# Performance work log

Measured on AMD Instinct MI355X. Metric: run time of the kernel, lower is better.

The kernel has to match this reference:

```python
import jax, jax.numpy as jnp
import numpy as np

DIM = 1028


def setup_inputs() -> dict:
    key = jax.random.key(0)
    ks = jax.random.split(key, 11)
    B, N = 8, 2048
    s = 0.02
    x = jax.random.normal(ks[0], (B, N, DIM), dtype=jnp.float32)
    Wq = jax.random.normal(ks[1], (DIM, DIM), dtype=jnp.float32) * s
    bq = jax.random.normal(ks[2], (DIM,), dtype=jnp.float32) * s
    Wk = jax.random.normal(ks[3], (DIM, DIM), dtype=jnp.float32) * s
    bk = jax.random.normal(ks[4], (DIM,), dtype=jnp.float32) * s
    Wv = jax.random.normal(ks[5], (DIM, DIM), dtype=jnp.float32) * s
    bv = jax.random.normal(ks[6], (DIM,), dtype=jnp.float32) * s
    We = jax.random.normal(ks[7], (4 * DIM, DIM), dtype=jnp.float32) * s
    be = jax.random.normal(ks[8], (4 * DIM,), dtype=jnp.float32) * s
    Wo = jax.random.normal(ks[9], (DIM, 4 * DIM), dtype=jnp.float32) * s
    bo = jax.random.normal(ks[10], (DIM,), dtype=jnp.float32) * s
    return {"x": x, "Wq": Wq, "bq": bq, "Wk": Wk, "bk": bk, "Wv": Wv,
            "bv": bv, "We": We, "be": be, "Wo": Wo, "bo": bo}


def reference(x, Wq, bq, Wk, bk, Wv, bv, We, be, Wo, bo):
    # x: [B, N, D]. torch Linear weight is [out, in] -> x @ W.T + b
    q = jnp.einsum('bnd,ed->bne', x, Wq) + bq
    k = jnp.einsum('bnd,ed->bne', x, Wk) + bk
    v = jnp.einsum('bnd,ed->bne', x, Wv) + bv
    scores = jnp.einsum('bqd,bkd->bqk', q, k) / jnp.sqrt(jnp.float32(DIM))
    w = jax.nn.softmax(scores, axis=-1)          # [B, N, N]
    attn = jnp.einsum('bqk,bkd->bqd', w, v)      # [B, N, D]
    h = jax.nn.gelu(jnp.einsum('bnd,hd->bnh', attn, We) + be, approximate=False)
    out = jnp.einsum('bnh,dh->bnd', h, Wo) + bo
    return out + x
```

## Files before the change

### kernel.cpp

```cpp
#include <hip/hip_runtime.h>
#include <hip/hip_bf16.h>
#include <cstdint>
#include <cmath>


typedef __bf16 bf16;
typedef __bf16 bf16x8 __attribute__((ext_vector_type(8)));
typedef float  f32x4  __attribute__((ext_vector_type(4)));

#define D_REAL   1028
#define D_PADK   1088
#define D_PADN   1152
#define H_REAL   4112
#define H_PAD    4224
#define NTOK     2048
#define NB       8
#define MTOT     (NB*NTOK)
#define SLAB_X   ((size_t)NTOK*D_PADK)
#define SLAB_S   ((size_t)NTOK*NTOK)
#define WSLAB    ((size_t)D_PADN*D_PADK)
#define VSLAB    ((size_t)D_PADN*NTOK)

__device__ __forceinline__ void async16(const void* g, void* l) {
    __builtin_amdgcn_global_load_lds(
        (__attribute__((address_space(1))) void*)(uintptr_t)g,
        (__attribute__((address_space(3))) void*)(uint32_t)(uintptr_t)l,
        16, 0, 0);
}

template <int EPI, bool XPIN>
__global__ __launch_bounds__(256)
void gemm_bt(const bf16* __restrict__ A, size_t strideA,
             const bf16* __restrict__ B, size_t strideB,
             const float* __restrict__ bias, size_t strideBias,
             void* __restrict__ Out, size_t strideOut,
             bf16* __restrict__ OutV,
             int K, int outPitch, int colBound, float scale,
             const float* __restrict__ resid)
{
    __shared__ __attribute__((aligned(16))) bf16 tA[128 * 64];
    __shared__ __attribute__((aligned(16))) bf16 tB[128 * 64];

    int bx, by, bz;
    if (XPIN) { bz = blockIdx.x; by = blockIdx.y; bx = blockIdx.z; }
    else      { bx = blockIdx.x; by = blockIdx.y; bz = blockIdx.z; }

    A += (size_t)bz * strideA;
    B += (size_t)bz * strideB;
    if (bias) bias += (size_t)bz * strideBias;

    const int tid  = threadIdx.x;
    const int lane = tid & 63;
    const int wv   = tid >> 6;
    const int wm   = wv >> 1;
    const int wn   = wv & 1;

    f32x4 acc[4][4] = {};

    const int sRow = lane >> 3;
    const int sCh  = (lane & 7) ^ sRow;
    const bf16* gA = A + (size_t)(by * 128 + wv * 32 + sRow) * K + sCh * 8;
    const bf16* gB = B + (size_t)(bx * 128 + wv * 32 + sRow) * K + sCh * 8;
    bf16* lA = &tA[(wv * 32) * 64];
    bf16* lB = &tB[(wv * 32) * 64];

    const int lr  = lane & 15;
    const int lq  = lane >> 4;
    const int rsw = lr & 7;

    for (int k0 = 0; k0 < K; k0 += 64) {
        async16(gA,                  lA);
        async16(gA + (size_t) 8 * K, lA +  8 * 64);
        async16(gA + (size_t)16 * K, lA + 16 * 64);
        async16(gA + (size_t)24 * K, lA + 24 * 64);
        async16(gB,                  lB);
        async16(gB + (size_t) 8 * K, lB +  8 * 64);
        async16(gB + (size_t)16 * K, lB + 16 * 64);
        async16(gB + (size_t)24 * K, lB + 24 * 64);
        gA += 64; gB += 64;
        __syncthreads();

        #pragma unroll
        for (int kk = 0; kk < 2; ++kk) {
            const int sl = ((kk * 4 + lq) ^ rsw) << 3;
            bf16x8 af[4], bfr[4];
            #pragma unroll
            for (int i = 0; i < 4; ++i) {
                af[i]  = *(const bf16x8*)&tA[(wm * 64 + i * 16 + lr) * 64 + sl];
                bfr[i] = *(const bf16x8*)&tB[(wn * 64 + i * 16 + lr) * 64 + sl];
            }
            #pragma unroll
            for (int i = 0; i < 4; ++i)
                #pragma unroll
                for (int j = 0; j < 4; ++j)
                    acc[i][j] = __builtin_amdgcn_mfma_f32_16x16x32_bf16(
                        af[i], bfr[j], acc[i][j], 0, 0, 0);
        }
        __syncthreads();
    }

    #pragma unroll
    for (int i = 0; i < 4; ++i) {
        #pragma unroll
        for (int j = 0; j < 4; ++j) {
            f32x4 v = acc[i][j];
            const int cg = bx * 128 + wn * 64 + j * 16 + lr;
            if (cg >= colBound) continue;
            const int rowBase = by * 128 + wm * 64 + i * 16 + lq * 4;
            const float bs = bias ? bias[cg] : 0.0f;
            #pragma unroll
            for (int r = 0; r < 4; ++r) {
                const int mg = rowBase + r;
                const float val = v[r];
                if (EPI == 0) {
                    ((bf16*)Out + (size_t)bz * strideOut)[(size_t)mg * outPitch + cg] =
                        (bf16)(val + bs);
                } else if (EPI == 3) {
                    const float u = val + bs;
                    const float g = 0.5f * u * (1.0f + erff(u * 0.70710678118654752f));
                    ((bf16*)Out)[(size_t)mg * outPitch + cg] = (bf16)g;
                } else if (EPI == 4) {
                    ((float*)Out)[(size_t)mg * outPitch + cg] =
                        val + bs + resid[(size_t)mg * outPitch + cg];
                } else if (EPI == 5) {
                    const int grp = cg / D_PADN;
                    const int c   = cg - grp * D_PADN;
                    const float u = val + bs;
                    if (grp < 2) {
                        if (c < D_PADK)
                            ((bf16*)Out)[(size_t)bz * 2 * SLAB_X + (size_t)grp * SLAB_X +
                                         (size_t)mg * D_PADK + c] = (bf16)u;
                    } else {
                        OutV[(size_t)bz * VSLAB + (size_t)c * NTOK + mg] = (bf16)u;
                    }
                } else {
                    ((bf16*)Out + (size_t)bz * strideOut)[(size_t)mg * outPitch + cg] =
                        (bf16)(val * scale);
                }
            }
        }
    }
}

__global__ __launch_bounds__(256)
void cvt_pad(const float* __restrict__ src, int R, int C,
             bf16* __restrict__ dst, int CP)
{
    const int c = blockIdx.x * 256 + threadIdx.x;
    const int r = blockIdx.y;
    if (c >= CP) return;
    const float v = (r < R && c < C) ? src[(size_t)r * C + c] : 0.0f;
    dst[(size_t)r * CP + c] = (bf16)v;
}

__global__ __launch_bounds__(256)
void pad_bias(const float* __restrict__ src, int n, float* __restrict__ dst, int np)
{
    const int i = blockIdx.x * 256 + threadIdx.x;
    if (i < np) dst[i] = (i < n) ? src[i] : 0.0f;
}

__global__ __launch_bounds__(256)
void softmax_ip(bf16* __restrict__ S)
{
    const int row  = blockIdx.x * 4 + (threadIdx.x >> 6);
    const int lane = threadIdx.x & 63;
    bf16* s = S + (size_t)row * NTOK + lane * 8;

    float v[32];
    #pragma unroll
    for (int j = 0; j < 4; ++j) {
        bf16x8 t = *(const bf16x8*)(s + j * 512);
        #pragma unroll
        for (int e = 0; e < 8; ++e) v[j * 8 + e] = (float)t[e];
    }
    float m = -1e30f;
    #pragma unroll
    for (int i = 0; i < 32; ++i) m = fmaxf(m, v[i]);
    #pragma unroll
    for (int off = 32; off > 0; off >>= 1) m = fmaxf(m, __shfl_xor(m, off, 64));

    float sum = 0.0f;
    #pragma unroll
    for (int i = 0; i < 32; ++i) { v[i] = __expf(v[i] - m); sum += v[i]; }
    #pragma unroll
    for (int off = 32; off > 0; off >>= 1) sum += __shfl_xor(sum, off, 64);
    const float inv = 1.0f / sum;

    #pragma unroll
    for (int j = 0; j < 4; ++j) {
        bf16x8 t;
        #pragma unroll
        for (int e = 0; e < 8; ++e) t[e] = (bf16)(v[j * 8 + e] * inv);
        *(bf16x8*)(s + j * 512) = t;
    }
}

#define OFF_WQKV   0u
#define OFF_WE     7520256u
#define OFF_WO     16711680u
#define OFF_BQKV   26443776u
#define OFF_BE     26457600u
#define OFF_XBF    26474496u
#define OFF_VT     62126080u
#define OFF_SCR    99874816u
#define QS_BYTES   8912896u
#define SS_BYTES   8388608u

extern "C" void kernel_launch(void* const* d_in, const int* in_sizes, int n_in,
                              void* d_out, int out_size, void* d_ws, size_t ws_size,
                              hipStream_t stream)
{
    const float* x  = (const float*)d_in[0];
    const float* Wq = (const float*)d_in[1];
    const float* bq = (const float*)d_in[2];
    const float* Wk = (const float*)d_in[3];
    const float* bk = (const float*)d_in[4];
    const float* Wv = (const float*)d_in[5];
    const float* bv = (const float*)d_in[6];
    const float* We = (const float*)d_in[7];
    const float* be = (const float*)d_in[8];
    const float* Wo = (const float*)d_in[9];
    const float* bo = (const float*)d_in[10];

    char* ws = (char*)d_ws;
    bf16*  Wqkv = (bf16*)(ws + OFF_WQKV);
    bf16*  WeP  = (bf16*)(ws + OFF_WE);
    bf16*  WoP  = (bf16*)(ws + OFF_WO);
    float* Bqkv = (float*)(ws + OFF_BQKV);
    float* BeP  = (float*)(ws + OFF_BE);
    bf16*  Xbf  = (bf16*)(ws + OFF_XBF);
    bf16*  Vt   = (bf16*)(ws + OFF_VT);
    char*  scr  = ws + OFF_SCR;

    const size_t avail = ws_size > OFF_SCR ? ws_size - OFF_SCR : 0;
    const size_t perG  = (size_t)QS_BYTES + SS_BYTES;
    int G = (avail >= 8 * perG) ? 8 : (avail >= 4 * perG) ? 4
          : (avail >= 2 * perG) ? 2 : 1;
    int R = (avail >= 69206016u) ? 8192 : (avail >= 34603008u) ? 4096 : 2048;

    bf16* Qs = (bf16*)scr;
    bf16* Ss = (bf16*)(scr + (size_t)G * QS_BYTES);
    bf16* Hb = (bf16*)scr;

    const dim3 blk(256);
    const float inv_sqrt_d = (float)(1.0 / sqrt((double)D_REAL));

    cvt_pad<<<dim3(5, MTOT), blk, 0, stream>>>(x, MTOT, D_REAL, Xbf, D_PADK);
    cvt_pad<<<dim3(5, D_PADN), blk, 0, stream>>>(Wq, D_REAL, D_REAL, Wqkv, D_PADK);
    cvt_pad<<<dim3(5, D_PADN), blk, 0, stream>>>(Wk, D_REAL, D_REAL, Wqkv + WSLAB, D_PADK);
    cvt_pad<<<dim3(5, D_PADN), blk, 0, stream>>>(Wv, D_REAL, D_REAL, Wqkv + 2 * WSLAB, D_PADK);
    cvt_pad<<<dim3(5, H_PAD), blk, 0, stream>>>(We, H_REAL, D_REAL, WeP, D_PADK);
    cvt_pad<<<dim3(17, D_PADN), blk, 0, stream>>>(Wo, D_REAL, H_REAL, WoP, H_PAD);
    pad_bias<<<dim3(5), blk, 0, stream>>>(bq, D_REAL, Bqkv, D_PADN);
    pad_bias<<<dim3(5), blk, 0, stream>>>(bk, D_REAL, Bqkv + D_PADN, D_PADN);
    pad_bias<<<dim3(5), blk, 0, stream>>>(bv, D_REAL, Bqkv + 2 * D_PADN, D_PADN);
    pad_bias<<<dim3(17), blk, 0, stream>>>(be, H_REAL, BeP, H_PAD);

    for (int g0 = 0; g0 < NB; g0 += G) {
        gemm_bt<5, false><<<dim3(27, 16, G), blk, 0, stream>>>(
            Xbf + (size_t)g0 * SLAB_X, SLAB_X, Wqkv, 0, Bqkv, 0,
            Qs, 0, Vt + (size_t)g0 * VSLAB,
            D_PADK, 0, 3456, 1.0f, nullptr);
        gemm_bt<6, true><<<dim3(G, 16, 16), blk, 0, stream>>>(
            Qs, 2 * SLAB_X, Qs + SLAB_X, 2 * SLAB_X, nullptr, 0,
            Ss, SLAB_S, nullptr, D_PADK, NTOK, NTOK, inv_sqrt_d, nullptr);
        softmax_ip<<<dim3(G * 512), blk, 0, stream>>>(Ss);
        gemm_bt<0, true><<<dim3(G, 16, 9), blk, 0, stream>>>(
            Ss, SLAB_S, Vt + (size_t)g0 * VSLAB, VSLAB, nullptr, 0,
            Xbf + (size_t)g0 * SLAB_X, SLAB_X, nullptr,
            NTOK, D_PADK, D_PADK, 1.0f, nullptr);
    }

    for (int r0 = 0; r0 < MTOT; r0 += R) {
        gemm_bt<3, false><<<dim3(33, R / 128, 1), blk, 0, stream>>>(
            Xbf + (size_t)r0 * D_PADK, 0, WeP, 0, BeP, 0,
            Hb, 0, nullptr, D_PADK, H_PAD, H_PAD, 1.0f, nullptr);
        gemm_bt<4, false><<<dim3(9, R / 128, 1), blk, 0, stream>>>(
            Hb, 0, WoP, 0, bo, 0,
            (float*)d_out + (size_t)r0 * D_REAL, 0, nullptr,
            H_PAD, D_REAL, D_REAL, 1.0f, x + (size_t)r0 * D_REAL);
    }
}
```

Baseline: 1.071 ms.

## Fuse softmax into score and PV GEMMs and remap blocks across XCDs

Removes the separate softmax pass. The QK^T GEMM now writes exp(scaled score) directly and atomically accumulates per-row sums, and the PV GEMM divides by the row sum in its epilogue. This avoids reading and writing the full score matrix once more. It also flattens all grids to 1D with a remap that groups contiguous logical tiles onto the same XCD (b&7) to improve L2 locality. Dropping the max subtraction risks overflow if scores are large, and the float atomics add nondeterminism.

```diff
diff --git a/kernel.cpp b/kernel.cpp
--- a/kernel.cpp
+++ b/kernel.cpp
@@ -28,22 +28,28 @@
         16, 0, 0);
 }
 
-template <int EPI, bool XPIN>
+template <int EPI>
 __global__ __launch_bounds__(256)
 void gemm_bt(const bf16* __restrict__ A, size_t strideA,
              const bf16* __restrict__ B, size_t strideB,
              const float* __restrict__ bias, size_t strideBias,
              void* __restrict__ Out, size_t strideOut,
-             bf16* __restrict__ OutV,
+             bf16* __restrict__ OutV, float* __restrict__ lsum,
              int K, int outPitch, int colBound, float scale,
-             const float* __restrict__ resid)
+             const float* __restrict__ resid, int gx, int gy)
 {
     __shared__ __attribute__((aligned(16))) bf16 tA[128 * 64];
     __shared__ __attribute__((aligned(16))) bf16 tB[128 * 64];
 
-    int bx, by, bz;
-    if (XPIN) { bz = blockIdx.x; by = blockIdx.y; bx = blockIdx.z; }
-    else      { bx = blockIdx.x; by = blockIdx.y; bz = blockIdx.z; }
+    {
+    }
+    const int T    = gridDim.x;
+    const int b    = blockIdx.x;
+    const int Lidx = (b & 7) * (T >> 3) + (b >> 3);
+    const int bx   = Lidx % gx;
+    const int t2   = Lidx / gx;
+    const int by   = t2 % gy;
+    const int bz   = t2 / gy;
 
     A += (size_t)bz * strideA;
     B += (size_t)bz * strideB;
@@ -99,23 +105,59 @@
         __syncthreads();
     }
 
+    if (EPI == 2) {
+        float rs[4][4] = {};
+        #pragma unroll
+        for (int i = 0; i < 4; ++i) {
+            const int rowBase = by * 128 + wm * 64 + i * 16 + lq * 4;
+            #pragma unroll
+            for (int j = 0; j < 4; ++j) {
+                const int cg = bx * 128 + wn * 64 + j * 16 + lr;
+                #pragma unroll
+                for (int r = 0; r < 4; ++r) {
+                    const float p = __expf(acc[i][j][r] * scale);
+                    ((bf16*)Out + (size_t)bz * strideOut)
+                        [(size_t)(rowBase + r) * outPitch + cg] = (bf16)p;
+                    rs[i][r] += p;
+                }
+            }
+        }
+        #pragma unroll
+        for (int i = 0; i < 4; ++i)
+            #pragma unroll
+            for (int r = 0; r < 4; ++r) {
+                float v = rs[i][r];
+                v += __shfl_xor(v, 1, 64);
+                v += __shfl_xor(v, 2, 64);
+                v += __shfl_xor(v, 4, 64);
+                v += __shfl_xor(v, 8, 64);
+                if (lr == 0)
+                    atomicAdd(&lsum[(size_t)bz * NTOK +
+                                    by * 128 + wm * 64 + i * 16 + lq * 4 + r], v);
+            }
+        return;
+    }
+
     #pragma unroll
     for (int i = 0; i < 4; ++i) {
+        const int rowBase = by * 128 + wm * 64 + i * 16 + lq * 4;
+        float invl[4];
+        if (EPI == 7) {
+            #pragma unroll
+            for (int r = 0; r < 4; ++r)
+                invl[r] = 1.0f / lsum[(size_t)bz * NTOK + rowBase + r];
+        }
         #pragma unroll
         for (int j = 0; j < 4; ++j) {
             f32x4 v = acc[i][j];
             const int cg = bx * 128 + wn * 64 + j * 16 + lr;
             if (cg >= colBound) continue;
-            const int rowBase = by * 128 + wm * 64 + i * 16 + lq * 4;
             const float bs = bias ? bias[cg] : 0.0f;
             #pragma unroll
             for (int r = 0; r < 4; ++r) {
                 const int mg = rowBase + r;
                 const float val = v[r];
-                if (EPI == 0) {
-                    ((bf16*)Out + (size_t)bz * strideOut)[(size_t)mg * outPitch + cg] =
-                        (bf16)(val + bs);
-                } else if (EPI == 3) {
+                if (EPI == 3) {
                     const float u = val + bs;
                     const float g = 0.5f * u * (1.0f + erff(u * 0.70710678118654752f));
                     ((bf16*)Out)[(size_t)mg * outPitch + cg] = (bf16)g;
@@ -135,7 +177,7 @@
                     }
                 } else {
                     ((bf16*)Out + (size_t)bz * strideOut)[(size_t)mg * outPitch + cg] =
-                        (bf16)(val * scale);
+                        (bf16)(val * invl[r]);
                 }
             }
         }
@@ -161,39 +203,10 @@
 }
 
 __global__ __launch_bounds__(256)
-void softmax_ip(bf16* __restrict__ S)
-{
-    const int row  = blockIdx.x * 4 + (threadIdx.x >> 6);
-    const int lane = threadIdx.x & 63;
-    bf16* s = S + (size_t)row * NTOK + lane * 8;
-
-    float v[32];
-    #pragma unroll
-    for (int j = 0; j < 4; ++j) {
-        bf16x8 t = *(const bf16x8*)(s + j * 512);
-        #pragma unroll
-        for (int e = 0; e < 8; ++e) v[j * 8 + e] = (float)t[e];
-    }
-    float m = -1e30f;
-    #pragma unroll
-    for (int i = 0; i < 32; ++i) m = fmaxf(m, v[i]);
-    #pragma unroll
-    for (int off = 32; off > 0; off >>= 1) m = fmaxf(m, __shfl_xor(m, off, 64));
-
-    float sum = 0.0f;
-    #pragma unroll
-    for (int i = 0; i < 32; ++i) { v[i] = __expf(v[i] - m); sum += v[i]; }
-    #pragma unroll
-    for (int off = 32; off > 0; off >>= 1) sum += __shfl_xor(sum, off, 64);
-    const float inv = 1.0f / sum;
-
-    #pragma unroll
-    for (int j = 0; j < 4; ++j) {
-        bf16x8 t;
-        #pragma unroll
-        for (int e = 0; e < 8; ++e) t[e] = (bf16)(v[j * 8 + e] * inv);
-        *(bf16x8*)(s + j * 512) = t;
-    }
+void zero_f32(float* __restrict__ p, int n)
+{
+    const int i = blockIdx.x * 256 + threadIdx.x;
+    if (i < n) p[i] = 0.0f;
 }
 
 #define OFF_WQKV   0u
@@ -201,9 +214,10 @@
 #define OFF_WO     16711680u
 #define OFF_BQKV   26443776u
 #define OFF_BE     26457600u
-#define OFF_XBF    26474496u
-#define OFF_VT     62126080u
-#define OFF_SCR    99874816u
+#define OFF_L      26474496u
+#define OFF_XBF    26540032u
+#define OFF_VT     62191616u
+#define OFF_SCR    99940352u
 #define QS_BYTES   8912896u
 #define SS_BYTES   8388608u
 
@@ -229,6 +243,7 @@
     bf16*  WoP  = (bf16*)(ws + OFF_WO);
     float* Bqkv = (float*)(ws + OFF_BQKV);
     float* BeP  = (float*)(ws + OFF_BE);
+    float* Lb   = (float*)(ws + OFF_L);
     bf16*  Xbf  = (bf16*)(ws + OFF_XBF);
     bf16*  Vt   = (bf16*)(ws + OFF_VT);
     char*  scr  = ws + OFF_SCR;
@@ -256,29 +271,31 @@
     pad_bias<<<dim3(5), blk, 0, stream>>>(bk, D_REAL, Bqkv + D_PADN, D_PADN);
     pad_bias<<<dim3(5), blk, 0, stream>>>(bv, D_REAL, Bqkv + 2 * D_PADN, D_PADN);
     pad_bias<<<dim3(17), blk, 0, stream>>>(be, H_REAL, BeP, H_PAD);
+    zero_f32<<<dim3(64), blk, 0, stream>>>(Lb, MTOT);
 
     for (int g0 = 0; g0 < NB; g0 += G) {
-        gemm_bt<5, false><<<dim3(27, 16, G), blk, 0, stream>>>(
+        gemm_bt<5><<<dim3(27 * 16 * G), blk, 0, stream>>>(
             Xbf + (size_t)g0 * SLAB_X, SLAB_X, Wqkv, 0, Bqkv, 0,
-            Qs, 0, Vt + (size_t)g0 * VSLAB,
-            D_PADK, 0, 3456, 1.0f, nullptr);
-        gemm_bt<6, true><<<dim3(G, 16, 16), blk, 0, stream>>>(
+            Qs, 0, Vt + (size_t)g0 * VSLAB, nullptr,
+            D_PADK, 0, 3456, 1.0f, nullptr, 27, 16);
+        gemm_bt<2><<<dim3(16 * 16 * G), blk, 0, stream>>>(
             Qs, 2 * SLAB_X, Qs + SLAB_X, 2 * SLAB_X, nullptr, 0,
-            Ss, SLAB_S, nullptr, D_PADK, NTOK, NTOK, inv_sqrt_d, nullptr);
-        softmax_ip<<<dim3(G * 512), blk, 0, stream>>>(Ss);
-        gemm_bt<0, true><<<dim3(G, 16, 9), blk, 0, stream>>>(
+            Ss, SLAB_S, nullptr, Lb + (size_t)g0 * NTOK,
+            D_PADK, NTOK, NTOK, inv_sqrt_d, nullptr, 16, 16);
+        gemm_bt<7><<<dim3(9 * 16 * G), blk, 0, stream>>>(
             Ss, SLAB_S, Vt + (size_t)g0 * VSLAB, VSLAB, nullptr, 0,
-            Xbf + (size_t)g0 * SLAB_X, SLAB_X, nullptr,
-            NTOK, D_PADK, D_PADK, 1.0f, nullptr);
+            Xbf + (size_t)g0 * SLAB_X, SLAB_X, nullptr, Lb + (size_t)g0 * NTOK,
+            NTOK, D_PADK, D_PADK, 1.0f, nullptr, 9, 16);
     }
 
     for (int r0 = 0; r0 < MTOT; r0 += R) {
-        gemm_bt<3, false><<<dim3(33, R / 128, 1), blk, 0, stream>>>(
+        gemm_bt<3><<<dim3(33 * (R / 128)), blk, 0, stream>>>(
             Xbf + (size_t)r0 * D_PADK, 0, WeP, 0, BeP, 0,
-            Hb, 0, nullptr, D_PADK, H_PAD, H_PAD, 1.0f, nullptr);
-        gemm_bt<4, false><<<dim3(9, R / 128, 1), blk, 0, stream>>>(
+            Hb, 0, nullptr, nullptr,
+            D_PADK, H_PAD, H_PAD, 1.0f, nullptr, 33, R / 128);
+        gemm_bt<4><<<dim3(9 * (R / 128)), blk, 0, stream>>>(
             Hb, 0, WoP, 0, bo, 0,
-            (float*)d_out + (size_t)r0 * D_REAL, 0, nullptr,
-            H_PAD, D_REAL, D_REAL, 1.0f, x + (size_t)r0 * D_REAL);
-    }
-}
+            (float*)d_out + (size_t)r0 * D_REAL, 0, nullptr, nullptr,
+            H_PAD, D_REAL, D_REAL, 1.0f, x + (size_t)r0 * D_REAL, 9, R / 128);
+    }
+}
```

Result: slower. 1.100 ms (+2.7%).
